# Performance work log

Hardware: AMD Instinct MI355X
Metric: run time of the kernel (lower is better)

Reference implementation:

```python
import jax, jax.numpy as jnp
import numpy as np

K_HOPS = 2  # number_layers


def _gcn_norm(edge_index, edge_weight, num_nodes):
    # add self loops with weight 1 (PyG gcn_norm default, fill_value=1)
    row, col = edge_index[0], edge_index[1]
    loop = jnp.arange(num_nodes, dtype=edge_index.dtype)
    row = jnp.concatenate([row, loop])
    col = jnp.concatenate([col, loop])
    w = jnp.concatenate([edge_weight, jnp.ones((num_nodes,), edge_weight.dtype)])
    deg = jax.ops.segment_sum(w, col, num_segments=num_nodes)
    dinv = jnp.where(deg > 0, jax.lax.rsqrt(deg), 0.0)
    norm = dinv[row] * w * dinv[col]
    return row, col, norm


def setup_inputs() -> dict:
    key = jax.random.key(0)
    k1, k2, k3, k4 = jax.random.split(key, 4)
    N, E, F_IN, F_OUT = 100000, 1600000, 256, 40
    x = jax.random.normal(k1, (N, F_IN), dtype=jnp.float32)
    edge_index = jax.random.randint(k2, (2, E), 0, N, dtype=jnp.int64)
    edge_attr = jax.random.uniform(k3, (E,), dtype=jnp.float32)
    W = jax.random.normal(k4, (F_OUT, F_IN), dtype=jnp.float32) * (1.0 / np.sqrt(F_IN))
    b = jnp.zeros((F_OUT,), dtype=jnp.float32)
    return {"x": x, "edge_index": edge_index, "edge_attr": edge_attr, "W": W, "b": b}


def reference(x, edge_index, edge_attr, W, b):
    N = x.shape[0]
    row, col, norm = _gcn_norm(edge_index, edge_attr, N)
    for _ in range(K_HOPS):
        x = jax.ops.segment_sum(norm[:, None] * x[row], col, num_segments=N)
    out = x @ W.T + b           # SGConv final linear
    out = jax.nn.relu(out)      # dropout is a no-op in eval mode
    return jax.nn.log_softmax(out, axis=-1)
```

## Files before the change

### kernel.cpp

```cpp
#include <hip/hip_runtime.h>
#include <hip/hip_bf16.h>
#include <math.h>

#define TF_IN   256
#define TF_OUT  40
#define NCH2    5
#define BCAP    48
#define WQ      32767.0f


struct us8 { ushort4 a, b; };

__device__ inline float bf2f(unsigned short u) {
    union { unsigned int i; float f; } t; t.i = ((unsigned int)u) << 16; return t.f;
}
__device__ inline unsigned short f2bf(float f) {
    union { float f; unsigned int i; } t; t.f = f;
    unsigned int r = t.i + 0x7FFF + ((t.i >> 16) & 1);
    return (unsigned short)(r >> 16);
}

__device__ inline void acc8(float* acc, float v, const us8& h) {
    acc[0] += v * bf2f(h.a.x); acc[1] += v * bf2f(h.a.y);
    acc[2] += v * bf2f(h.a.z); acc[3] += v * bf2f(h.a.w);
    acc[4] += v * bf2f(h.b.x); acc[5] += v * bf2f(h.b.y);
    acc[6] += v * bf2f(h.b.z); acc[7] += v * bf2f(h.b.w);
}

__global__ void zero_kernel(int* __restrict__ cnt, int N) {
    int i = blockIdx.x * blockDim.x + threadIdx.x;
    if (i < N) cnt[i] = 0;
}

__global__ __launch_bounds__(256) void fused_gemm_scatter_kernel(
        const float* __restrict__ x, const float* __restrict__ W,
        unsigned short* __restrict__ h, int N, int gemmBlocks, int R,
        const int* __restrict__ row, const int* __restrict__ col,
        const float* __restrict__ w, int* __restrict__ cnt,
        unsigned int* __restrict__ bucket, int E) {
    __shared__ float4 xs[128][8];
    __shared__ float4 wsm[40][9];
    int tid = threadIdx.x;
    int b = blockIdx.x;
    int q = b / (R + 1);
    int r = b - q * (R + 1);

    if (r == R) {
        int ng = tid >> 2;
        int jg = tid & 3;
        int j0 = jg * 10;
        int nodeBase = q * 128;
        int sk = (ng >> 1) & 7;

        float acc[2][10];
#pragma unroll
        for (int i = 0; i < 2; ++i)
#pragma unroll
            for (int j = 0; j < 10; ++j) acc[i][j] = 0.f;

        const float4* x4 = (const float4*)x;
        const float4* W4 = (const float4*)W;

        for (int kt = 0; kt < 8; ++kt) {
            int kb4 = kt * 8;
#pragma unroll
            for (int i = 0; i < 4; ++i) {
                int idx = tid + i * 256;
                int n = idx >> 3, c4 = idx & 7;
                int gn = nodeBase + n;
                float4 v = make_float4(0.f, 0.f, 0.f, 0.f);
                if (gn < N) v = x4[(size_t)gn * (TF_IN / 4) + kb4 + c4];
                xs[n][c4 ^ ((n >> 2) & 7)] = v;
            }
            {
                int idx = tid;
                int j = idx >> 3, c4 = idx & 7;
                wsm[j][c4] = W4[(size_t)j * (TF_IN / 4) + kb4 + c4];
                if (tid < 64) {
                    idx = tid + 256;
                    j = idx >> 3; c4 = idx & 7;
                    wsm[j][c4] = W4[(size_t)j * (TF_IN / 4) + kb4 + c4];
                }
            }
            __syncthreads();
#pragma unroll 2
            for (int c4 = 0; c4 < 8; ++c4) {
                int phys = c4 ^ sk;
                float4 xv0 = xs[ng * 2][phys];
                float4 xv1 = xs[ng * 2 + 1][phys];
#pragma unroll
                for (int jj = 0; jj < 10; ++jj) {
                    float4 wv = wsm[j0 + jj][c4];
                    acc[0][jj] += xv0.x * wv.x + xv0.y * wv.y + xv0.z * wv.z + xv0.w * wv.w;
                    acc[1][jj] += xv1.x * wv.x + xv1.y * wv.y + xv1.z * wv.z + xv1.w * wv.w;
                }
            }
            __syncthreads();
        }

#pragma unroll
        for (int i = 0; i < 2; ++i) {
            int gn = nodeBase + ng * 2 + i;
            if (gn < N) {
                ushort2* hp2 = (ushort2*)(h + (size_t)gn * TF_OUT + j0);
#pragma unroll
                for (int p = 0; p < 5; ++p) {
                    ushort2 o;
                    o.x = f2bf(acc[i][2 * p]);
                    o.y = f2bf(acc[i][2 * p + 1]);
                    hp2[p] = o;
                }
            }
        }
    } else {
        int sIdx = q * R + r;
        int e = sIdx * 256 + tid;
        if (e < E) {
            int c = col[e];
            int pos = atomicAdd(&cnt[c], 1);
            if (pos < BCAP) {
                unsigned int wq = (unsigned int)(w[e] * WQ + 0.5f);
                bucket[(size_t)c * BCAP + pos] = ((unsigned int)row[e] << 15) | wq;
            }
        }
    }
}

__global__ void deg_kernel(const unsigned int* __restrict__ bucket, const int* __restrict__ cnt,
                           float* __restrict__ dinv, int N) {
    int n = blockIdx.x * blockDim.x + threadIdx.x;
    if (n >= N) return;
    int m = cnt[n]; if (m > BCAP) m = BCAP;
    const unsigned int* b = bucket + (size_t)n * BCAP;
    unsigned int si = 0;
    int k = 0;
    for (; k + 4 <= m; k += 4) {
        uint4 e4 = *(const uint4*)(b + k);
        si += (e4.x & 0x7FFF) + (e4.y & 0x7FFF) + (e4.z & 0x7FFF) + (e4.w & 0x7FFF);
    }
    for (; k < m; ++k) si += b[k] & 0x7FFF;
    float s = 1.0f + (float)si * (1.0f / WQ);
    dinv[n] = rsqrtf(s);
}

__device__ inline void stage_rv(int g, int chunk, int m,
                                const unsigned int* __restrict__ b,
                                const float* __restrict__ dinv,
                                int rs[64][BCAP + 1], float vs[64][BCAP + 1]) {
    int k0 = chunk * 10;
    unsigned int e[10];
#pragma unroll
    for (int i = 0; i < 10; ++i) {
        int k = k0 + i;
        e[i] = (k < m) ? b[k] : 0u;
    }
    float dv[10];
#pragma unroll
    for (int i = 0; i < 10; ++i) dv[i] = dinv[e[i] >> 15];
#pragma unroll
    for (int i = 0; i < 10; ++i) {
        int k = k0 + i;
        if (k < m) {
            rs[g][k] = (int)(e[i] >> 15);
            vs[g][k] = dv[i] * ((float)(e[i] & 0x7FFF) * (1.0f / WQ));
        }
    }
}

__device__ inline void gather_lds(float* acc, const us8* __restrict__ hin,
                                  int g, int chunk, int m,
                                  const int rs[64][BCAP + 1], const float vs[64][BCAP + 1]) {
    int k = 0;
    for (; k + 4 <= m; k += 4) {
        int r0 = rs[g][k],     r1 = rs[g][k + 1];
        int r2 = rs[g][k + 2], r3 = rs[g][k + 3];
        us8 h0 = hin[(size_t)r0 * NCH2 + chunk];
        us8 h1 = hin[(size_t)r1 * NCH2 + chunk];
        us8 h2 = hin[(size_t)r2 * NCH2 + chunk];
        us8 h3 = hin[(size_t)r3 * NCH2 + chunk];
        acc8(acc, vs[g][k],     h0); acc8(acc, vs[g][k + 1], h1);
        acc8(acc, vs[g][k + 2], h2); acc8(acc, vs[g][k + 3], h3);
    }
    for (; k < m; ++k) {
        us8 hv = hin[(size_t)rs[g][k] * NCH2 + chunk];
        acc8(acc, vs[g][k], hv);
    }
}

__global__ __launch_bounds__(320) void hop_bf_kernel(
        const us8* __restrict__ hin, us8* __restrict__ hout,
        const int* __restrict__ cnt, const unsigned int* __restrict__ bucket,
        const float* __restrict__ dinv, int N) {
    __shared__ int   rs[64][BCAP + 1];
    __shared__ float vs[64][BCAP + 1];
    int tid = threadIdx.x;
    int g = tid / NCH2;
    int chunk = tid - g * NCH2;
    int node = blockIdx.x * 64 + g;

    int m = 0;
    float d = 0.f;
    if (node < N) {
        m = cnt[node]; if (m > BCAP) m = BCAP;
        d = dinv[node];
        stage_rv(g, chunk, m, bucket + (size_t)node * BCAP, dinv, rs, vs);
    }
    __syncthreads();
    if (node >= N) return;

    us8 a = hin[(size_t)node * NCH2 + chunk];
    float acc[8];
    acc[0] = bf2f(a.a.x) * d; acc[1] = bf2f(a.a.y) * d;
    acc[2] = bf2f(a.a.z) * d; acc[3] = bf2f(a.a.w) * d;
    acc[4] = bf2f(a.b.x) * d; acc[5] = bf2f(a.b.y) * d;
    acc[6] = bf2f(a.b.z) * d; acc[7] = bf2f(a.b.w) * d;

    gather_lds(acc, hin, g, chunk, m, rs, vs);

    us8 o;
    o.a.x = f2bf(acc[0] * d); o.a.y = f2bf(acc[1] * d);
    o.a.z = f2bf(acc[2] * d); o.a.w = f2bf(acc[3] * d);
    o.b.x = f2bf(acc[4] * d); o.b.y = f2bf(acc[5] * d);
    o.b.z = f2bf(acc[6] * d); o.b.w = f2bf(acc[7] * d);
    hout[(size_t)node * NCH2 + chunk] = o;
}

__global__ __launch_bounds__(320) void hop2_epi_kernel(
        const us8* __restrict__ hin, float4* __restrict__ out,
        const int* __restrict__ cnt, const unsigned int* __restrict__ bucket,
        const float* __restrict__ dinv, const float* __restrict__ bias, int N) {
    __shared__ int   rs[64][BCAP + 1];
    __shared__ float vs[64][BCAP + 1];
    __shared__ float redm[320];
    __shared__ float reds[320];
    int tid = threadIdx.x;
    int g = tid / NCH2;
    int chunk = tid - g * NCH2;
    int node = blockIdx.x * 64 + g;
    bool valid = node < N;

    int m = 0;
    float d = 0.f;
    if (valid) {
        m = cnt[node]; if (m > BCAP) m = BCAP;
        d = dinv[node];
        stage_rv(g, chunk, m, bucket + (size_t)node * BCAP, dinv, rs, vs);
    }
    __syncthreads();

    float acc[8];
#pragma unroll
    for (int j = 0; j < 8; ++j) acc[j] = 0.f;
    if (valid) {
        us8 a = hin[(size_t)node * NCH2 + chunk];
        acc[0] = bf2f(a.a.x) * d; acc[1] = bf2f(a.a.y) * d;
        acc[2] = bf2f(a.a.z) * d; acc[3] = bf2f(a.a.w) * d;
        acc[4] = bf2f(a.b.x) * d; acc[5] = bf2f(a.b.y) * d;
        acc[6] = bf2f(a.b.z) * d; acc[7] = bf2f(a.b.w) * d;
        gather_lds(acc, hin, g, chunk, m, rs, vs);
    }

    float v[8];
    float lm = -1e30f;
    if (valid) {
#pragma unroll
        for (int j = 0; j < 8; ++j) {
            float t2 = acc[j] * d + bias[chunk * 8 + j];
            t2 = fmaxf(t2, 0.f);
            v[j] = t2;
            lm = fmaxf(lm, t2);
        }
    }
    redm[tid] = lm;
    __syncthreads();
    float gm = redm[g * NCH2];
#pragma unroll
    for (int i = 1; i < NCH2; ++i) gm = fmaxf(gm, redm[g * NCH2 + i]);

    float ps = 0.f;
    if (valid) {
#pragma unroll
        for (int j = 0; j < 8; ++j) ps += __expf(v[j] - gm);
    }
    reds[tid] = ps;
    __syncthreads();
    float s = reds[g * NCH2];
#pragma unroll
    for (int i = 1; i < NCH2; ++i) s += reds[g * NCH2 + i];
    float lse = gm + __logf(s);

    if (valid) {
        float4 o0 = make_float4(v[0] - lse, v[1] - lse, v[2] - lse, v[3] - lse);
        float4 o1 = make_float4(v[4] - lse, v[5] - lse, v[6] - lse, v[7] - lse);
        out[(size_t)node * 10 + chunk * 2]     = o0;
        out[(size_t)node * 10 + chunk * 2 + 1] = o1;
    }
}

extern "C" void kernel_launch(void* const* d_in, const int* in_sizes, int n_in,
                              void* d_out, int out_size, void* d_ws, size_t ws_size,
                              hipStream_t stream) {
    const float* x  = (const float*)d_in[0];
    const int*   ei = (const int*)d_in[1];
    const float* ew = (const float*)d_in[2];
    const float* W  = (const float*)d_in[3];
    const float* b  = (const float*)d_in[4];

    const int F_out = in_sizes[4];
    const int F_in  = in_sizes[3] / F_out;
    const int N     = in_sizes[0] / F_in;
    const int E     = in_sizes[2];
    const int* row = ei;
    const int* col = ei + E;

    char* ws = (char*)d_ws;
    size_t off = 0;
    auto alloc = [&](size_t bytes) {
        void* p = ws + off;
        off += (bytes + 255) & ~(size_t)255;
        return p;
    };

    int*          cnt    = (int*)          alloc((size_t)N * 4);
    float*        dinv   = (float*)        alloc((size_t)N * 4);
    unsigned int* bucket = (unsigned int*) alloc((size_t)N * BCAP * 4);
    unsigned short* h0   = (unsigned short*)alloc((size_t)N * TF_OUT * 2);
    unsigned short* h1   = (unsigned short*)alloc((size_t)N * TF_OUT * 2);

    const int tb = 256;
    hipLaunchKernelGGL(zero_kernel, dim3((N + tb - 1) / tb), dim3(tb), 0, stream, cnt, N);

    int gemmBlocks    = (N + 127) / 128;
    int scatterBlocks = (E + 255) / 256;
    int R             = (scatterBlocks + gemmBlocks - 1) / gemmBlocks;
    hipLaunchKernelGGL(fused_gemm_scatter_kernel, dim3((R + 1) * gemmBlocks), dim3(256),
                       0, stream, x, W, h0, N, gemmBlocks, R, row, col, ew, cnt, bucket, E);

    hipLaunchKernelGGL(deg_kernel, dim3((N + tb - 1) / tb), dim3(tb), 0, stream,
                       bucket, cnt, dinv, N);

    int hopBlocks = (N + 63) / 64;
    hipLaunchKernelGGL(hop_bf_kernel, dim3(hopBlocks), dim3(320), 0, stream,
                       (const us8*)h0, (us8*)h1, cnt, bucket, dinv, N);

    hipLaunchKernelGGL(hop2_epi_kernel, dim3(hopBlocks), dim3(320), 0, stream,
                       (const us8*)h1, (float4*)d_out, cnt, bucket, dinv, b, N);
}
```

Baseline: 346.0 us.

## Pre-bin edges by destination range before scattering into per-node buckets

Adds a first pass that groups edges into coarse bins of 256 destination nodes, using the output buffer as scratch. The fused GEMM kernel then has each scatter block drain one bin, so the per-node atomics and bucket writes hit a small, cache-resident region instead of random addresses across the whole bucket array. In exchange it adds an extra kernel and an extra read/write of all edges, and the binning atomics hit only a few hundred counters, so contention there is high. Edges past a fixed bin capacity would be dropped.

```diff
diff --git a/kernel.cpp b/kernel.cpp
--- a/kernel.cpp
+++ b/kernel.cpp
@@ -7,6 +7,7 @@
 #define NCH2    5
 #define BCAP    48
 #define WQ      32767.0f
+#define BIN_SHIFT 8
 
 
 struct us8 { ushort4 a, b; };
@@ -27,25 +28,64 @@
     acc[6] += v * bf2f(h.b.z); acc[7] += v * bf2f(h.b.w);
 }
 
-__global__ void zero_kernel(int* __restrict__ cnt, int N) {
+__global__ void zero_kernel(int* __restrict__ a, int na, int* __restrict__ b, int nb) {
     int i = blockIdx.x * blockDim.x + threadIdx.x;
-    if (i < N) cnt[i] = 0;
-}
-
-__global__ __launch_bounds__(256) void fused_gemm_scatter_kernel(
+    if (i < na) a[i] = 0;
+    if (i < nb) b[i] = 0;
+}
+
+__device__ inline void bin_one(int c, int r, float wv,
+                               int* __restrict__ binCnt, uint2* __restrict__ bins,
+                               int bincap) {
+    int b = c >> BIN_SHIFT;
+    int pos = atomicAdd(&binCnt[b], 1);
+    if (pos < bincap) {
+        unsigned int wq = (unsigned int)(wv * WQ + 0.5f);
+        uint2 e; e.x = ((unsigned int)r << 15) | wq; e.y = (unsigned int)c;
+        bins[(size_t)b * bincap + pos] = e;
+    }
+}
+
+__global__ __launch_bounds__(256) void bin_kernel(
+        const int* __restrict__ row, const int* __restrict__ col,
+        const float* __restrict__ w, int* __restrict__ binCnt,
+        uint2* __restrict__ bins, int E, int bincap) {
+    int base = (blockIdx.x * 256 + threadIdx.x) * 4;
+    if (base + 4 <= E) {
+        int4   c4 = *(const int4*)(col + base);
+        int4   r4 = *(const int4*)(row + base);
+        float4 w4 = *(const float4*)(w + base);
+        bin_one(c4.x, r4.x, w4.x, binCnt, bins, bincap);
+        bin_one(c4.y, r4.y, w4.y, binCnt, bins, bincap);
+        bin_one(c4.z, r4.z, w4.z, binCnt, bins, bincap);
+        bin_one(c4.w, r4.w, w4.w, binCnt, bins, bincap);
+    } else {
+        for (int e = base; e < E; ++e)
+            bin_one(col[e], row[e], w[e], binCnt, bins, bincap);
+    }
+}
+
+__global__ __launch_bounds__(256) void fused_gemm_binscatter_kernel(
         const float* __restrict__ x, const float* __restrict__ W,
-        unsigned short* __restrict__ h, int N, int gemmBlocks, int R,
-        const int* __restrict__ row, const int* __restrict__ col,
-        const float* __restrict__ w, int* __restrict__ cnt,
-        unsigned int* __restrict__ bucket, int E) {
+        unsigned short* __restrict__ h, int N, int nbins,
+        const int* __restrict__ binCnt, const uint2* __restrict__ bins, int bincap,
+        int* __restrict__ cnt, unsigned int* __restrict__ bucket) {
     __shared__ float4 xs[128][8];
     __shared__ float4 wsm[40][9];
     int tid = threadIdx.x;
-    int b = blockIdx.x;
-    int q = b / (R + 1);
-    int r = b - q * (R + 1);
-
-    if (r == R) {
+
+    if ((int)blockIdx.x < nbins) {
+        int b = blockIdx.x;
+        int mb = binCnt[b]; if (mb > bincap) mb = bincap;
+        const uint2* src = bins + (size_t)b * bincap;
+        for (int i = tid; i < mb; i += 256) {
+            uint2 e = src[i];
+            int c = (int)e.y;
+            int pos = atomicAdd(&cnt[c], 1);
+            if (pos < BCAP) bucket[(size_t)c * BCAP + pos] = e.x;
+        }
+    } else {
+        int q = (int)blockIdx.x - nbins;
         int ng = tid >> 2;
         int jg = tid & 3;
         int j0 = jg * 10;
@@ -112,17 +152,6 @@
                 }
             }
         }
-    } else {
-        int sIdx = q * R + r;
-        int e = sIdx * 256 + tid;
-        if (e < E) {
-            int c = col[e];
-            int pos = atomicAdd(&cnt[c], 1);
-            if (pos < BCAP) {
-                unsigned int wq = (unsigned int)(w[e] * WQ + 0.5f);
-                bucket[(size_t)c * BCAP + pos] = ((unsigned int)row[e] << 15) | wq;
-            }
-        }
     }
 }
 
@@ -326,15 +355,24 @@
     unsigned int* bucket = (unsigned int*) alloc((size_t)N * BCAP * 4);
     unsigned short* h0   = (unsigned short*)alloc((size_t)N * TF_OUT * 2);
     unsigned short* h1   = (unsigned short*)alloc((size_t)N * TF_OUT * 2);
+    int nbins = (N + (1 << BIN_SHIFT) - 1) >> BIN_SHIFT;
+    int* binCnt = (int*)alloc((size_t)nbins * 4);
+
+    size_t outBytes = (size_t)N * F_out * 4;
+    int bincap = (int)(outBytes / ((size_t)nbins * 8));
+    uint2* bins = (uint2*)d_out;
 
     const int tb = 256;
-    hipLaunchKernelGGL(zero_kernel, dim3((N + tb - 1) / tb), dim3(tb), 0, stream, cnt, N);
-
-    int gemmBlocks    = (N + 127) / 128;
-    int scatterBlocks = (E + 255) / 256;
-    int R             = (scatterBlocks + gemmBlocks - 1) / gemmBlocks;
-    hipLaunchKernelGGL(fused_gemm_scatter_kernel, dim3((R + 1) * gemmBlocks), dim3(256),
-                       0, stream, x, W, h0, N, gemmBlocks, R, row, col, ew, cnt, bucket, E);
+    hipLaunchKernelGGL(zero_kernel, dim3((N + tb - 1) / tb), dim3(tb), 0, stream,
+                       cnt, N, binCnt, nbins);
+
+    int binBlocks = (E / 4 + tb - 1) / tb;
+    hipLaunchKernelGGL(bin_kernel, dim3(binBlocks), dim3(tb), 0, stream,
+                       row, col, ew, binCnt, bins, E, bincap);
+
+    int gemmBlocks = (N + 127) / 128;
+    hipLaunchKernelGGL(fused_gemm_binscatter_kernel, dim3(nbins + gemmBlocks), dim3(256),
+                       0, stream, x, W, h0, N, nbins, binCnt, bins, bincap, cnt, bucket);
 
     hipLaunchKernelGGL(deg_kernel, dim3((N + tb - 1) / tb), dim3(tb), 0, stream,
                        bucket, cnt, dinv, N);
```

Result: slower. 868.7 us (+151.1%).
